# Performance work log

Measured on AMD Instinct MI355X. Metric: run time of the kernel, lower is better.

Reference implementation:

```python
import jax, jax.numpy as jnp
import numpy as np

DIM = 1028


def setup_inputs() -> dict:
    key = jax.random.key(0)
    ks = jax.random.split(key, 11)
    B, N = 8, 2048
    s = 0.02
    x = jax.random.normal(ks[0], (B, N, DIM), dtype=jnp.float32)
    Wq = jax.random.normal(ks[1], (DIM, DIM), dtype=jnp.float32) * s
    bq = jax.random.normal(ks[2], (DIM,), dtype=jnp.float32) * s
    Wk = jax.random.normal(ks[3], (DIM, DIM), dtype=jnp.float32) * s
    bk = jax.random.normal(ks[4], (DIM,), dtype=jnp.float32) * s
    Wv = jax.random.normal(ks[5], (DIM, DIM), dtype=jnp.float32) * s
    bv = jax.random.normal(ks[6], (DIM,), dtype=jnp.float32) * s
    We = jax.random.normal(ks[7], (4 * DIM, DIM), dtype=jnp.float32) * s
    be = jax.random.normal(ks[8], (4 * DIM,), dtype=jnp.float32) * s
    Wo = jax.random.normal(ks[9], (DIM, 4 * DIM), dtype=jnp.float32) * s
    bo = jax.random.normal(ks[10], (DIM,), dtype=jnp.float32) * s
    return {"x": x, "Wq": Wq, "bq": bq, "Wk": Wk, "bk": bk, "Wv": Wv,
            "bv": bv, "We": We, "be": be, "Wo": Wo, "bo": bo}


def reference(x, Wq, bq, Wk, bk, Wv, bv, We, be, Wo, bo):
    # x: [B, N, D]. torch Linear weight is [out, in] -> x @ W.T + b
    q = jnp.einsum('bnd,ed->bne', x, Wq) + bq
    k = jnp.einsum('bnd,ed->bne', x, Wk) + bk
    v = jnp.einsum('bnd,ed->bne', x, Wv) + bv
    scores = jnp.einsum('bqd,bkd->bqk', q, k) / jnp.sqrt(jnp.float32(DIM))
    w = jax.nn.softmax(scores, axis=-1)          # [B, N, N]
    attn = jnp.einsum('bqk,bkd->bqd', w, v)      # [B, N, D]
    h = jax.nn.gelu(jnp.einsum('bnd,hd->bnh', attn, We) + be, approximate=False)
    out = jnp.einsum('bnh,dh->bnd', h, Wo) + bo
    return out + x
```

## Files before the change

kernel.cpp:

```cpp
#include <hip/hip_runtime.h>
#include <hip/hip_bf16.h>
#include <cstdint>
#include <cmath>


typedef __bf16 bf16;
typedef __bf16 bf16x8 __attribute__((ext_vector_type(8)));
typedef float  f32x4  __attribute__((ext_vector_type(4)));

#define D_REAL   1028
#define D_PADK   1088
#define D_PADN   1152
#define H_REAL   4112
#define H_PAD    4224
#define NTOK     2048
#define NB       8
#define MTOT     (NB*NTOK)
#define SLAB_X   ((size_t)NTOK*D_PADK)
#define SLAB_S   ((size_t)NTOK*NTOK)
#define WSLAB    ((size_t)D_PADN*D_PADK)
#define VSLAB    ((size_t)D_PADN*NTOK)

__device__ __forceinline__ void async16(const void* g, void* l) {
    __builtin_amdgcn_global_load_lds(
        (__attribute__((address_space(1))) void*)(uintptr_t)g,
        (__attribute__((address_space(3))) void*)(uint32_t)(uintptr_t)l,
        16, 0, 0);
}

template <int EPI, bool XPIN>
__global__ __launch_bounds__(256, 4)
void gemm_bt(const bf16* __restrict__ A, size_t strideA,
             const bf16* __restrict__ B, size_t strideB,
             const float* __restrict__ bias, size_t strideBias,
             void* __restrict__ Out, size_t strideOut,
             bf16* __restrict__ OutV,
             int K, int outPitch, int colBound, float scale,
             const float* __restrict__ resid)
{
    __shared__ __attribute__((aligned(16))) bf16 tA[128 * 64];
    __shared__ __attribute__((aligned(16))) bf16 tB[128 * 64];

    int bx, by, bz;
    if (XPIN) { bz = blockIdx.x; by = blockIdx.y; bx = blockIdx.z; }
    else      { bx = blockIdx.x; by = blockIdx.y; bz = blockIdx.z; }

    A += (size_t)bz * strideA;
    B += (size_t)bz * strideB;
    if (bias) bias += (size_t)bz * strideBias;

    const int tid  = threadIdx.x;
    const int lane = tid & 63;
    const int wv   = tid >> 6;
    const int wm   = wv >> 1;
    const int wn   = wv & 1;

    f32x4 acc[4][4] = {};

    const int sRow = lane >> 3;
    const int sCh  = (lane & 7) ^ sRow;
    const bf16* gA = A + (size_t)(by * 128 + wv * 32 + sRow) * K + sCh * 8;
    const bf16* gB = B + (size_t)(bx * 128 + wv * 32 + sRow) * K + sCh * 8;
    bf16* lA = &tA[(wv * 32) * 64];
    bf16* lB = &tB[(wv * 32) * 64];

    const int lr  = lane & 15;
    const int lq  = lane >> 4;
    const int rsw = lr & 7;

    for (int k0 = 0; k0 < K; k0 += 64) {
        async16(gA,                  lA);
        async16(gA + (size_t) 8 * K, lA +  8 * 64);
        async16(gA + (size_t)16 * K, lA + 16 * 64);
        async16(gA + (size_t)24 * K, lA + 24 * 64);
        async16(gB,                  lB);
        async16(gB + (size_t) 8 * K, lB +  8 * 64);
        async16(gB + (size_t)16 * K, lB + 16 * 64);
        async16(gB + (size_t)24 * K, lB + 24 * 64);
        gA += 64; gB += 64;
        __syncthreads();

        #pragma unroll
        for (int kk = 0; kk < 2; ++kk) {
            const int sl = ((kk * 4 + lq) ^ rsw) << 3;
            bf16x8 bfr[4];
            #pragma unroll
            for (int j = 0; j < 4; ++j)
                bfr[j] = *(const bf16x8*)&tB[(wn * 64 + j * 16 + lr) * 64 + sl];
            #pragma unroll
            for (int i = 0; i < 4; ++i) {
                const bf16x8 af = *(const bf16x8*)&tA[(wm * 64 + i * 16 + lr) * 64 + sl];
                #pragma unroll
                for (int j = 0; j < 4; ++j)
                    acc[i][j] = __builtin_amdgcn_mfma_f32_16x16x32_bf16(
                        af, bfr[j], acc[i][j], 0, 0, 0);
            }
        }
        __syncthreads();
    }

    #pragma unroll
    for (int i = 0; i < 4; ++i) {
        #pragma unroll
        for (int j = 0; j < 4; ++j) {
            f32x4 v = acc[i][j];
            const int cg = bx * 128 + wn * 64 + j * 16 + lr;
            if (cg >= colBound) continue;
            const int rowBase = by * 128 + wm * 64 + i * 16 + lq * 4;
            const float bs = bias ? bias[cg] : 0.0f;
            #pragma unroll
            for (int r = 0; r < 4; ++r) {
                const int mg = rowBase + r;
                const float val = v[r];
                if (EPI == 0) {
                    ((bf16*)Out + (size_t)bz * strideOut)[(size_t)mg * outPitch + cg] =
                        (bf16)(val + bs);
                } else if (EPI == 3) {
                    const float u = val + bs;
                    const float g = 0.5f * u * (1.0f + erff(u * 0.70710678118654752f));
                    ((bf16*)Out)[(size_t)mg * outPitch + cg] = (bf16)g;
                } else if (EPI == 4) {
                    ((float*)Out)[(size_t)mg * outPitch + cg] =
                        val + bs + resid[(size_t)mg * outPitch + cg];
                } else if (EPI == 5) {
                    const int grp = cg / D_PADN;
                    const int c   = cg - grp * D_PADN;
                    const float u = val + bs;
                    if (grp < 2) {
                        if (c < D_PADK)
                            ((bf16*)Out)[(size_t)bz * 2 * SLAB_X + (size_t)grp * SLAB_X +
                                         (size_t)mg * D_PADK + c] = (bf16)u;
                    } else {
                        OutV[(size_t)bz * VSLAB + (size_t)c * NTOK + mg] = (bf16)u;
                    }
                } else {
                    ((bf16*)Out + (size_t)bz * strideOut)[(size_t)mg * outPitch + cg] =
                        (bf16)(val * scale);
                }
            }
        }
    }
}

__global__ __launch_bounds__(256)
void cvt_pad(const float* __restrict__ src, int R, int C,
             bf16* __restrict__ dst, int CP)
{
    const int c = blockIdx.x * 256 + threadIdx.x;
    const int r = blockIdx.y;
    if (c >= CP) return;
    const float v = (r < R && c < C) ? src[(size_t)r * C + c] : 0.0f;
    dst[(size_t)r * CP + c] = (bf16)v;
}

__global__ __launch_bounds__(256)
void pad_bias(const float* __restrict__ src, int n, float* __restrict__ dst, int np)
{
    const int i = blockIdx.x * 256 + threadIdx.x;
    if (i < np) dst[i] = (i < n) ? src[i] : 0.0f;
}

__global__ __launch_bounds__(256)
void softmax_ip(bf16* __restrict__ S)
{
    const int row  = blockIdx.x * 4 + (threadIdx.x >> 6);
    const int lane = threadIdx.x & 63;
    bf16* s = S + (size_t)row * NTOK + lane * 8;

    float v[32];
    #pragma unroll
    for (int j = 0; j < 4; ++j) {
        bf16x8 t = *(const bf16x8*)(s + j * 512);
        #pragma unroll
        for (int e = 0; e < 8; ++e) v[j * 8 + e] = (float)t[e];
    }
    float m = -1e30f;
    #pragma unroll
    for (int i = 0; i < 32; ++i) m = fmaxf(m, v[i]);
    #pragma unroll
    for (int off = 32; off > 0; off >>= 1) m = fmaxf(m, __shfl_xor(m, off, 64));

    float sum = 0.0f;
    #pragma unroll
    for (int i = 0; i < 32; ++i) { v[i] = __expf(v[i] - m); sum += v[i]; }
    #pragma unroll
    for (int off = 32; off > 0; off >>= 1) sum += __shfl_xor(sum, off, 64);
    const float inv = 1.0f / sum;

    #pragma unroll
    for (int j = 0; j < 4; ++j) {
        bf16x8 t;
        #pragma unroll
        for (int e = 0; e < 8; ++e) t[e] = (bf16)(v[j * 8 + e] * inv);
        *(bf16x8*)(s + j * 512) = t;
    }
}

#define OFF_WQKV   0u
#define OFF_WE     7520256u
#define OFF_WO     16711680u
#define OFF_BQKV   26443776u
#define OFF_BE     26457600u
#define OFF_XBF    26474496u
#define OFF_VT     62126080u
#define OFF_SCR    99874816u
#define QS_BYTES   8912896u
#define SS_BYTES   8388608u

extern "C" void kernel_launch(void* const* d_in, const int* in_sizes, int n_in,
                              void* d_out, int out_size, void* d_ws, size_t ws_size,
                              hipStream_t stream)
{
    const float* x  = (const float*)d_in[0];
    const float* Wq = (const float*)d_in[1];
    const float* bq = (const float*)d_in[2];
    const float* Wk = (const float*)d_in[3];
    const float* bk = (const float*)d_in[4];
    const float* Wv = (const float*)d_in[5];
    const float* bv = (const float*)d_in[6];
    const float* We = (const float*)d_in[7];
    const float* be = (const float*)d_in[8];
    const float* Wo = (const float*)d_in[9];
    const float* bo = (const float*)d_in[10];

    char* ws = (char*)d_ws;
    bf16*  Wqkv = (bf16*)(ws + OFF_WQKV);
    bf16*  WeP  = (bf16*)(ws + OFF_WE);
    bf16*  WoP  = (bf16*)(ws + OFF_WO);
    float* Bqkv = (float*)(ws + OFF_BQKV);
    float* BeP  = (float*)(ws + OFF_BE);
    bf16*  Xbf  = (bf16*)(ws + OFF_XBF);
    bf16*  Vt   = (bf16*)(ws + OFF_VT);
    char*  scr  = ws + OFF_SCR;

    const size_t avail = ws_size > OFF_SCR ? ws_size - OFF_SCR : 0;
    const size_t perG  = (size_t)QS_BYTES + SS_BYTES;
    int G = (avail >= 8 * perG) ? 8 : (avail >= 4 * perG) ? 4
          : (avail >= 2 * perG) ? 2 : 1;
    int R = (avail >= 69206016u) ? 8192 : (avail >= 34603008u) ? 4096 : 2048;

    bf16* Qs = (bf16*)scr;
    bf16* Ss = (bf16*)(scr + (size_t)G * QS_BYTES);
    bf16* Hb = (bf16*)scr;

    const dim3 blk(256);
    const float inv_sqrt_d = (float)(1.0 / sqrt((double)D_REAL));

    cvt_pad<<<dim3(5, MTOT), blk, 0, stream>>>(x, MTOT, D_REAL, Xbf, D_PADK);
    cvt_pad<<<dim3(5, D_PADN), blk, 0, stream>>>(Wq, D_REAL, D_REAL, Wqkv, D_PADK);
    cvt_pad<<<dim3(5, D_PADN), blk, 0, stream>>>(Wk, D_REAL, D_REAL, Wqkv + WSLAB, D_PADK);
    cvt_pad<<<dim3(5, D_PADN), blk, 0, stream>>>(Wv, D_REAL, D_REAL, Wqkv + 2 * WSLAB, D_PADK);
    cvt_pad<<<dim3(5, H_PAD), blk, 0, stream>>>(We, H_REAL, D_REAL, WeP, D_PADK);
    cvt_pad<<<dim3(17, D_PADN), blk, 0, stream>>>(Wo, D_REAL, H_REAL, WoP, H_PAD);
    pad_bias<<<dim3(5), blk, 0, stream>>>(bq, D_REAL, Bqkv, D_PADN);
    pad_bias<<<dim3(5), blk, 0, stream>>>(bk, D_REAL, Bqkv + D_PADN, D_PADN);
    pad_bias<<<dim3(5), blk, 0, stream>>>(bv, D_REAL, Bqkv + 2 * D_PADN, D_PADN);
    pad_bias<<<dim3(17), blk, 0, stream>>>(be, H_REAL, BeP, H_PAD);

    for (int g0 = 0; g0 < NB; g0 += G) {
        gemm_bt<5, false><<<dim3(27, 16, G), blk, 0, stream>>>(
            Xbf + (size_t)g0 * SLAB_X, SLAB_X, Wqkv, 0, Bqkv, 0,
            Qs, 0, Vt + (size_t)g0 * VSLAB,
            D_PADK, 0, 3456, 1.0f, nullptr);
        gemm_bt<6, true><<<dim3(G, 16, 16), blk, 0, stream>>>(
            Qs, 2 * SLAB_X, Qs + SLAB_X, 2 * SLAB_X, nullptr, 0,
            Ss, SLAB_S, nullptr, D_PADK, NTOK, NTOK, inv_sqrt_d, nullptr);
        softmax_ip<<<dim3(G * 512), blk, 0, stream>>>(Ss);
        gemm_bt<0, true><<<dim3(G, 16, 9), blk, 0, stream>>>(
            Ss, SLAB_S, Vt + (size_t)g0 * VSLAB, VSLAB, nullptr, 0,
            Xbf + (size_t)g0 * SLAB_X, SLAB_X, nullptr,
            NTOK, D_PADK, D_PADK, 1.0f, nullptr);
    }

    for (int r0 = 0; r0 < MTOT; r0 += R) {
        gemm_bt<3, false><<<dim3(33, R / 128, 1), blk, 0, stream>>>(
            Xbf + (size_t)r0 * D_PADK, 0, WeP, 0, BeP, 0,
            Hb, 0, nullptr, D_PADK, H_PAD, H_PAD, 1.0f, nullptr);
        gemm_bt<4, false><<<dim3(9, R / 128, 1), blk, 0, stream>>>(
            Hb, 0, WoP, 0, bo, 0,
            (float*)d_out + (size_t)r0 * D_REAL, 0, nullptr,
            H_PAD, D_REAL, D_REAL, 1.0f, x + (size_t)r0 * D_REAL);
    }
}
```

Baseline: 1.077 ms.

## Add 256x128-tile GEMM variant with workgroup remapping for QKV and expansion GEMMs

Result: slower. 1.258 ms (+16.8%).

```diff
diff --git a/kernel.cpp b/kernel.cpp
--- a/kernel.cpp
+++ b/kernel.cpp
@@ -28,6 +28,41 @@
         16, 0, 0);
 }
 
+template <int EPI>
+__device__ __forceinline__ void epi_store(
+    float val, int mg, int cg, int bz,
+    const float* __restrict__ bias, void* __restrict__ Out, size_t strideOut,
+    bf16* __restrict__ OutV, int outPitch, float scale,
+    const float* __restrict__ resid)
+{
+    const float bs = bias ? bias[cg] : 0.0f;
+    if (EPI == 0) {
+        ((bf16*)Out + (size_t)bz * strideOut)[(size_t)mg * outPitch + cg] =
+            (bf16)(val + bs);
+    } else if (EPI == 3) {
+        const float u = val + bs;
+        const float g = 0.5f * u * (1.0f + erff(u * 0.70710678118654752f));
+        ((bf16*)Out)[(size_t)mg * outPitch + cg] = (bf16)g;
+    } else if (EPI == 4) {
+        ((float*)Out)[(size_t)mg * outPitch + cg] =
+            val + bs + resid[(size_t)mg * outPitch + cg];
+    } else if (EPI == 5) {
+        const int grp = cg / D_PADN;
+        const int c   = cg - grp * D_PADN;
+        const float u = val + bs;
+        if (grp < 2) {
+            if (c < D_PADK)
+                ((bf16*)Out)[(size_t)bz * 2 * SLAB_X + (size_t)grp * SLAB_X +
+                             (size_t)mg * D_PADK + c] = (bf16)u;
+        } else {
+            OutV[(size_t)bz * VSLAB + (size_t)c * NTOK + mg] = (bf16)u;
+        }
+    } else {
+        ((bf16*)Out + (size_t)bz * strideOut)[(size_t)mg * outPitch + cg] =
+            (bf16)(val * scale);
+    }
+}
+
 template <int EPI, bool XPIN>
 __global__ __launch_bounds__(256, 4)
 void gemm_bt(const bf16* __restrict__ A, size_t strideA,
@@ -107,37 +142,108 @@
             const int cg = bx * 128 + wn * 64 + j * 16 + lr;
             if (cg >= colBound) continue;
             const int rowBase = by * 128 + wm * 64 + i * 16 + lq * 4;
-            const float bs = bias ? bias[cg] : 0.0f;
-            #pragma unroll
-            for (int r = 0; r < 4; ++r) {
-                const int mg = rowBase + r;
-                const float val = v[r];
-                if (EPI == 0) {
-                    ((bf16*)Out + (size_t)bz * strideOut)[(size_t)mg * outPitch + cg] =
-                        (bf16)(val + bs);
-                } else if (EPI == 3) {
-                    const float u = val + bs;
-                    const float g = 0.5f * u * (1.0f + erff(u * 0.70710678118654752f));
-                    ((bf16*)Out)[(size_t)mg * outPitch + cg] = (bf16)g;
-                } else if (EPI == 4) {
-                    ((float*)Out)[(size_t)mg * outPitch + cg] =
-                        val + bs + resid[(size_t)mg * outPitch + cg];
-                } else if (EPI == 5) {
-                    const int grp = cg / D_PADN;
-                    const int c   = cg - grp * D_PADN;
-                    const float u = val + bs;
-                    if (grp < 2) {
-                        if (c < D_PADK)
-                            ((bf16*)Out)[(size_t)bz * 2 * SLAB_X + (size_t)grp * SLAB_X +
-                                         (size_t)mg * D_PADK + c] = (bf16)u;
-                    } else {
-                        OutV[(size_t)bz * VSLAB + (size_t)c * NTOK + mg] = (bf16)u;
-                    }
-                } else {
-                    ((bf16*)Out + (size_t)bz * strideOut)[(size_t)mg * outPitch + cg] =
-                        (bf16)(val * scale);
-                }
+            #pragma unroll
+            for (int r = 0; r < 4; ++r)
+                epi_store<EPI>(v[r], rowBase + r, cg, bz, bias, Out, strideOut,
+                               OutV, outPitch, scale, resid);
+        }
+    }
+}
+
+template <int EPI, bool XPIN>
+__global__ __launch_bounds__(256, 2)
+void gemm_btw(const bf16* __restrict__ A, size_t strideA,
+              const bf16* __restrict__ B, size_t strideB,
+              const float* __restrict__ bias, size_t strideBias,
+              void* __restrict__ Out, size_t strideOut,
+              bf16* __restrict__ OutV,
+              int K, int outPitch, int colBound, float scale,
+              const float* __restrict__ resid)
+{
+    __shared__ __attribute__((aligned(16))) bf16 tA[256 * 64];
+    __shared__ __attribute__((aligned(16))) bf16 tB[128 * 64];
+
+    int bx, by, bz;
+    if (XPIN) { bz = blockIdx.x; by = blockIdx.y; bx = blockIdx.z; }
+    else {
+        const int nx   = gridDim.x;
+        const int nwg  = nx * gridDim.y;
+        const int orig = blockIdx.y * nx + blockIdx.x;
+        const int q    = nwg >> 3;
+        const int wg   = (orig & 7) * q + (orig >> 3);
+        bx = wg % nx; by = wg / nx; bz = blockIdx.z;
+    }
+
+    A += (size_t)bz * strideA;
+    B += (size_t)bz * strideB;
+    if (bias) bias += (size_t)bz * strideBias;
+
+    const int tid  = threadIdx.x;
+    const int lane = tid & 63;
+    const int wv   = tid >> 6;
+    const int wm   = wv >> 1;
+    const int wn   = wv & 1;
+
+    f32x4 acc[8][4] = {};
+
+    const int sRow = lane >> 3;
+    const int sCh  = (lane & 7) ^ sRow;
+    const bf16* gA = A + (size_t)(by * 256 + wv * 64 + sRow) * K + sCh * 8;
+    const bf16* gB = B + (size_t)(bx * 128 + wv * 32 + sRow) * K + sCh * 8;
+    bf16* lA = &tA[(wv * 64) * 64];
+    bf16* lB = &tB[(wv * 32) * 64];
+
+    const int lr  = lane & 15;
+    const int lq  = lane >> 4;
+    const int rsw = lr & 7;
+
+    for (int k0 = 0; k0 < K; k0 += 64) {
+        async16(gA,                  lA);
+        async16(gA + (size_t) 8 * K, lA +  8 * 64);
+        async16(gA + (size_t)16 * K, lA + 16 * 64);
+        async16(gA + (size_t)24 * K, lA + 24 * 64);
+        async16(gA + (size_t)32 * K, lA + 32 * 64);
+        async16(gA + (size_t)40 * K, lA + 40 * 64);
+        async16(gA + (size_t)48 * K, lA + 48 * 64);
+        async16(gA + (size_t)56 * K, lA + 56 * 64);
+        async16(gB,                  lB);
+        async16(gB + (size_t) 8 * K, lB +  8 * 64);
+        async16(gB + (size_t)16 * K, lB + 16 * 64);
+        async16(gB + (size_t)24 * K, lB + 24 * 64);
+        gA += 64; gB += 64;
+        __syncthreads();
+
+        #pragma unroll
+        for (int kk = 0; kk < 2; ++kk) {
+            const int sl = ((kk * 4 + lq) ^ rsw) << 3;
+            bf16x8 bfr[4];
+            #pragma unroll
+            for (int j = 0; j < 4; ++j)
+                bfr[j] = *(const bf16x8*)&tB[(wn * 64 + j * 16 + lr) * 64 + sl];
+            #pragma unroll
+            for (int i = 0; i < 8; ++i) {
+                const bf16x8 af = *(const bf16x8*)&tA[(wm * 128 + i * 16 + lr) * 64 + sl];
+                #pragma unroll
+                for (int j = 0; j < 4; ++j)
+                    acc[i][j] = __builtin_amdgcn_mfma_f32_16x16x32_bf16(
+                        af, bfr[j], acc[i][j], 0, 0, 0);
             }
+        }
+        __syncthreads();
+    }
+
+    #pragma unroll
+    for (int i = 0; i < 8; ++i) {
+        #pragma unroll
+        for (int j = 0; j < 4; ++j) {
+            f32x4 v = acc[i][j];
+            const int cg = bx * 128 + wn * 64 + j * 16 + lr;
+            if (cg >= colBound) continue;
+            const int rowBase = by * 256 + wm * 128 + i * 16 + lq * 4;
+            #pragma unroll
+            for (int r = 0; r < 4; ++r)
+                epi_store<EPI>(v[r], rowBase + r, cg, bz, bias, Out, strideOut,
+                               OutV, outPitch, scale, resid);
         }
     }
 }
@@ -258,7 +364,7 @@
     pad_bias<<<dim3(17), blk, 0, stream>>>(be, H_REAL, BeP, H_PAD);
 
     for (int g0 = 0; g0 < NB; g0 += G) {
-        gemm_bt<5, false><<<dim3(27, 16, G), blk, 0, stream>>>(
+        gemm_btw<5, false><<<dim3(27, 8, G), blk, 0, stream>>>(
             Xbf + (size_t)g0 * SLAB_X, SLAB_X, Wqkv, 0, Bqkv, 0,
             Qs, 0, Vt + (size_t)g0 * VSLAB,
             D_PADK, 0, 3456, 1.0f, nullptr);
@@ -273,7 +379,7 @@
     }
 
     for (int r0 = 0; r0 < MTOT; r0 += R) {
-        gemm_bt<3, false><<<dim3(33, R / 128, 1), blk, 0, stream>>>(
+        gemm_btw<3, false><<<dim3(33, R / 256, 1), blk, 0, stream>>>(
             Xbf + (size_t)r0 * D_PADK, 0, WeP, 0, BeP, 0,
             Hb, 0, nullptr, D_PADK, H_PAD, H_PAD, 1.0f, nullptr);
         gemm_bt<4, false><<<dim3(9, R / 128, 1), blk, 0, stream>>>(
```
